# Optimization experiments

Measured on AMD Instinct MI355X. Metric: run time of the kernel, lower is better.

## Reference

```python
import jax, jax.numpy as jnp
import numpy as np

N_NODES = 50000
N_EDGES = 800000
F = 64      # node feature channels (irreps_out = 64x0e)
L = 4       # edge spherical-harmonic dim (lmax=1)
R = 8       # radial basis size
H = 64      # radial MLP hidden
AVG_NUM_NEIGHBOURS = 16.0


def setup_inputs() -> dict:
    key = jax.random.key(0)
    ks = jax.random.split(key, 10)
    node_features = jax.random.normal(ks[0], (N_NODES, F), jnp.float32)
    edge_features = jax.random.normal(ks[1], (N_EDGES, L), jnp.float32)
    radial_embedding = jax.random.uniform(ks[2], (N_EDGES, R), jnp.float32)
    senders = jax.random.randint(ks[3], (N_EDGES,), 0, N_NODES)
    receivers = jax.random.randint(ks[4], (N_EDGES,), 0, N_NODES)
    edge_mask = jnp.ones((N_EDGES,), jnp.bool_)
    W_up = jax.random.normal(ks[5], (F, F), jnp.float32) / np.sqrt(F)
    W1 = jax.random.normal(ks[6], (R, H), jnp.float32) / np.sqrt(R)
    W2 = jax.random.normal(ks[7], (H, H), jnp.float32) / np.sqrt(H)
    W3 = jax.random.normal(ks[8], (H, F * L), jnp.float32) / np.sqrt(H)
    W_down = jax.random.normal(ks[9], (F, F), jnp.float32) / np.sqrt(F)
    return dict(node_features=node_features, edge_features=edge_features,
                radial_embedding=radial_embedding, senders=senders,
                receivers=receivers, edge_mask=edge_mask,
                W_up=W_up, W1=W1, W2=W2, W3=W3, W_down=W_down)


def reference(node_features, edge_features, radial_embedding, senders,
              receivers, edge_mask, W_up, W1, W2, W3, W_down):
    n_nodes = node_features.shape[0]
    # linear_up
    x = node_features @ W_up  # [N, F]
    # radial MLP -> per-edge, per-(channel, l) tensor-product path weights
    h = jax.nn.swish(radial_embedding @ W1)
    h = jax.nn.swish(h @ W2)
    w = (h @ W3).reshape(-1, F, L)  # [E, F, L]
    # gather sender features, weighted tensor product with edge attrs,
    # contracted over the edge-attribute (spherical-harmonic) axis
    x_s = x[senders]  # [E, F]
    msg = jnp.einsum('ef,el,efl->ef', x_s, edge_features, w)  # [E, F]
    msg = jnp.where(edge_mask[:, None], msg, jnp.zeros((), msg.dtype))
    # scatter-add to receivers and normalize
    agg = jax.ops.segment_sum(msg, receivers, num_segments=n_nodes)
    agg = agg / AVG_NUM_NEIGHBOURS
    # linear_down
    return agg @ W_down
```

## Files before the change

kernel.cpp:

```cpp
#include <hip/hip_runtime.h>
#include <hip/hip_bf16.h>

typedef _Float16 half8 __attribute__((ext_vector_type(8)));
typedef _Float16 half4v __attribute__((ext_vector_type(4)));
typedef float f32x4 __attribute__((ext_vector_type(4)));

#define NN 50000
#define NE 800000

__device__ __forceinline__ float swishf(float v) {
  return v * __builtin_amdgcn_rcpf(1.f + __expf(-v));
}

__global__ __launch_bounds__(256)
void prep_kernel(const float* __restrict__ nf, const float* __restrict__ W_up,
                 _Float16* __restrict__ xbuf, const int* __restrict__ rcv,
                 int* __restrict__ deg, const float* __restrict__ W3,
                 const float* __restrict__ W2, _Float16* __restrict__ w3p,
                 _Float16* __restrict__ w2p) {
  const int b = blockIdx.x, tid = threadIdx.x;
  if (b < 12500) {
    const int gid = b * 256 + tid;
    const int row = gid >> 6, lane = tid & 63;
    const float* xr = nf + (long)row * 64;
    float acc = 0.f;
#pragma unroll
    for (int k = 0; k < 64; ++k) acc = fmaf(xr[k], W_up[k * 64 + lane], acc);
    xbuf[(long)row * 64 + lane] = (_Float16)acc;
  } else if (b < 15625) {
    const int e = (b - 12500) * 256 + tid;
    atomicAdd(&deg[rcv[e]], 1);
  } else {
    const int bb = b - 15625;
    if (bb < 8) {
      int t = bb * 256 + tid;
      int lane = t & 63, nt = (t >> 6) & 3, ks = t >> 8;
      int f = 16 * nt + (lane & 15);
      int jb = 32 * ks + 8 * (lane >> 4);
#pragma unroll
      for (int u = 0; u < 8; ++u) {
        int j = jb + u;
        w3p[t * 8 + u] = (_Float16)W3[(j >> 2) * 256 + 4 * f + (j & 3)];
      }
    } else {
      int t = (bb - 8) * 256 + tid;
      if (t < 512) {
        int lane = t & 63, nt = (t >> 6) & 3, kk = t >> 8;
        int c = 16 * nt + (lane & 15);
        int kb = 32 * kk + 8 * (lane >> 4);
#pragma unroll
        for (int u = 0; u < 8; ++u)
          w2p[t * 8 + u] = (_Float16)W2[(kb + u) * 64 + c];
      }
    }
  }
}

__global__ __launch_bounds__(256)
void scan1_kernel(const int* __restrict__ deg, int* __restrict__ bsum) {
  __shared__ int s[256];
  int gid = blockIdx.x * 256 + threadIdx.x;
  s[threadIdx.x] = (gid < NN) ? deg[gid] : 0;
  __syncthreads();
  for (int d = 128; d > 0; d >>= 1) {
    if (threadIdx.x < d) s[threadIdx.x] += s[threadIdx.x + d];
    __syncthreads();
  }
  if (threadIdx.x == 0) bsum[blockIdx.x] = s[0];
}

__global__ __launch_bounds__(256)
void scan2_kernel(const int* __restrict__ bsum, int* __restrict__ boff) {
  __shared__ int s[256];
  int t = threadIdx.x;
  int v = (t < 196) ? bsum[t] : 0;
  s[t] = v;
  __syncthreads();
  for (int d = 1; d < 256; d <<= 1) {
    int x = (t >= d) ? s[t - d] : 0;
    __syncthreads();
    s[t] += x;
    __syncthreads();
  }
  boff[t] = s[t] - v;
}

__global__ __launch_bounds__(256)
void scan3_kernel(const int* __restrict__ deg, const int* __restrict__ boff,
                  int* __restrict__ pos, int* __restrict__ cur) {
  __shared__ int s[256];
  int t = threadIdx.x, gid = blockIdx.x * 256 + t;
  int v = (gid < NN) ? deg[gid] : 0;
  s[t] = v;
  __syncthreads();
  for (int d = 1; d < 256; d <<= 1) {
    int x = (t >= d) ? s[t - d] : 0;
    __syncthreads();
    s[t] += x;
    __syncthreads();
  }
  int ex = s[t] - v + boff[blockIdx.x];
  if (gid < NN) {
    pos[gid] = ex;
    cur[gid] = ex;
    if (gid == NN - 1) pos[NN] = ex + v;
  }
}

__global__ __launch_bounds__(256, 4)
void fused_tp_kernel(const float* __restrict__ rad, const float* __restrict__ ef,
                     const _Float16* __restrict__ xup, const int* __restrict__ snd,
                     const int* __restrict__ rcv, const int* __restrict__ msk,
                     const float* __restrict__ W1,
                     const _Float16* __restrict__ w2p, const _Float16* __restrict__ w3p,
                     int* __restrict__ cur, _Float16* __restrict__ msg) {
  __shared__ float    s_ef[128][4];
  __shared__ _Float16 s_xs[128][72];
  __shared__ _Float16 s_hp[128][72];
  __shared__ int      s_slot[128];

  const int t = threadIdx.x;
  const long e0 = (long)blockIdx.x * 128;
  const int w = t >> 6, lane = t & 63, m = lane & 15, g = lane >> 4;
  const int ew0 = 32 * w;

  {
    const float2 e2 = *reinterpret_cast<const float2*>(ef + (e0 + ew0) * 4 + lane * 2);
    const int rr = ew0 + (lane >> 1), rc = 2 * (lane & 1);
    s_ef[rr][rc] = e2.x;
    s_ef[rr][rc + 1] = e2.y;
    if (lane < 32) s_slot[ew0 + lane] = atomicAdd(&cur[rcv[e0 + ew0 + lane]], 1);
    const int e = ew0 + (lane >> 1), q2 = lane & 1;
    const int sn = snd[e0 + e];
    const int mk = msk[e0 + e];
    uint4 v0 = {0,0,0,0}, v1 = {0,0,0,0}, v2 = {0,0,0,0}, v3 = {0,0,0,0};
    if (mk) {
      const uint4* src = reinterpret_cast<const uint4*>(xup + (long)sn * 64 + q2 * 32);
      v0 = src[0]; v1 = src[1]; v2 = src[2]; v3 = src[3];
    }
    uint4* dst = reinterpret_cast<uint4*>(&s_xs[e][q2 * 32]);
    dst[0] = v0; dst[1] = v1; dst[2] = v2; dst[3] = v3;
  }

  const int em0 = ew0 + m;
  const int em1 = ew0 + 16 + m;

  float rv0[8], rv1[8];
  {
    const float4 a = *reinterpret_cast<const float4*>(rad + (e0 + em0) * 8);
    const float4 b = *reinterpret_cast<const float4*>(rad + (e0 + em0) * 8 + 4);
    const float4 c = *reinterpret_cast<const float4*>(rad + (e0 + em1) * 8);
    const float4 d = *reinterpret_cast<const float4*>(rad + (e0 + em1) * 8 + 4);
    rv0[0]=a.x; rv0[1]=a.y; rv0[2]=a.z; rv0[3]=a.w;
    rv0[4]=b.x; rv0[5]=b.y; rv0[6]=b.z; rv0[7]=b.w;
    rv1[0]=c.x; rv1[1]=c.y; rv1[2]=c.z; rv1[3]=c.w;
    rv1[4]=d.x; rv1[5]=d.y; rv1[6]=d.z; rv1[7]=d.w;
  }

  half8 af0[2], af1[2];
#pragma unroll
  for (int kk = 0; kk < 2; ++kk) {
    float a0[8], a1[8];
#pragma unroll
    for (int u = 0; u < 8; ++u) { a0[u] = 0.f; a1[u] = 0.f; }
#pragma unroll
    for (int k = 0; k < 8; ++k) {
      const float4 wa = *reinterpret_cast<const float4*>(W1 + k * 64 + 32 * kk + 8 * g);
      const float4 wb = *reinterpret_cast<const float4*>(W1 + k * 64 + 32 * kk + 8 * g + 4);
      a0[0] = fmaf(rv0[k], wa.x, a0[0]);  a1[0] = fmaf(rv1[k], wa.x, a1[0]);
      a0[1] = fmaf(rv0[k], wa.y, a0[1]);  a1[1] = fmaf(rv1[k], wa.y, a1[1]);
      a0[2] = fmaf(rv0[k], wa.z, a0[2]);  a1[2] = fmaf(rv1[k], wa.z, a1[2]);
      a0[3] = fmaf(rv0[k], wa.w, a0[3]);  a1[3] = fmaf(rv1[k], wa.w, a1[3]);
      a0[4] = fmaf(rv0[k], wb.x, a0[4]);  a1[4] = fmaf(rv1[k], wb.x, a1[4]);
      a0[5] = fmaf(rv0[k], wb.y, a0[5]);  a1[5] = fmaf(rv1[k], wb.y, a1[5]);
      a0[6] = fmaf(rv0[k], wb.z, a0[6]);  a1[6] = fmaf(rv1[k], wb.z, a1[6]);
      a0[7] = fmaf(rv0[k], wb.w, a0[7]);  a1[7] = fmaf(rv1[k], wb.w, a1[7]);
    }
#pragma unroll
    for (int u = 0; u < 8; ++u) {
      af0[kk][u] = (_Float16)swishf(a0[u]);
      af1[kk][u] = (_Float16)swishf(a1[u]);
    }
  }

  {
    half8 bw[8];
#pragma unroll
    for (int i = 0; i < 8; ++i)
      bw[i] = *reinterpret_cast<const half8*>(w2p + ((size_t)i * 64 + lane) * 8);

    f32x4 A0[4], A1[4];
#pragma unroll
    for (int nt = 0; nt < 4; ++nt) { A0[nt] = (f32x4){0.f,0.f,0.f,0.f}; A1[nt] = (f32x4){0.f,0.f,0.f,0.f}; }
#pragma unroll
    for (int kk = 0; kk < 2; ++kk) {
#pragma unroll
      for (int nt = 0; nt < 4; ++nt) {
        A0[nt] = __builtin_amdgcn_mfma_f32_16x16x32_f16(af0[kk], bw[kk * 4 + nt], A0[nt], 0, 0, 0);
        A1[nt] = __builtin_amdgcn_mfma_f32_16x16x32_f16(af1[kk], bw[kk * 4 + nt], A1[nt], 0, 0, 0);
      }
    }
    const int col = lane & 15, rg = lane >> 4;
    const int pbase = 16 * ((col >> 1) & 3) + 2 * (col >> 3) + (col & 1);
#pragma unroll
    for (int nt = 0; nt < 4; ++nt) {
      const int pos = pbase + 4 * nt;
#pragma unroll
      for (int i = 0; i < 4; ++i) {
        const int r0 = ew0 + rg * 4 + i;
        s_hp[r0][pos]      = (_Float16)swishf(A0[nt][i]);
        s_hp[r0 + 16][pos] = (_Float16)swishf(A1[nt][i]);
      }
    }
  }

  {
    const _Float16* hr0 = &s_hp[em0][g * 16];
    const _Float16* hr1 = &s_hp[em1][g * 16];
    half8 hlo0 = *reinterpret_cast<const half8*>(hr0);
    half8 hhi0 = *reinterpret_cast<const half8*>(hr0 + 8);
    half8 hlo1 = *reinterpret_cast<const half8*>(hr1);
    half8 hhi1 = *reinterpret_cast<const half8*>(hr1 + 8);

    _Float16 ef0[4], ef1[4];
#pragma unroll
    for (int l = 0; l < 4; ++l) {
      ef0[l] = (_Float16)s_ef[em0][l];
      ef1[l] = (_Float16)s_ef[em1][l];
    }

    f32x4 c0[4], c1[4];
#pragma unroll
    for (int nt = 0; nt < 4; ++nt) { c0[nt] = (f32x4){0.f,0.f,0.f,0.f}; c1[nt] = (f32x4){0.f,0.f,0.f,0.f}; }

#pragma unroll
    for (int ks = 0; ks < 8; ++ks) {
      half8 bfr[4];
#pragma unroll
      for (int nt = 0; nt < 4; ++nt)
        bfr[nt] = *reinterpret_cast<const half8*>(w3p + ((size_t)(ks * 4 + nt) * 64 + lane) * 8);

      const _Float16 p0  = (ks < 4) ? hlo0[2 * ks]     : hhi0[2 * (ks - 4)];
      const _Float16 p1  = (ks < 4) ? hlo0[2 * ks + 1] : hhi0[2 * (ks - 4) + 1];
      const _Float16 q0  = (ks < 4) ? hlo1[2 * ks]     : hhi1[2 * (ks - 4)];
      const _Float16 q1  = (ks < 4) ? hlo1[2 * ks + 1] : hhi1[2 * (ks - 4) + 1];
      half8 a0, a1;
#pragma unroll
      for (int l = 0; l < 4; ++l) {
        a0[l]     = p0 * ef0[l];
        a0[4 + l] = p1 * ef0[l];
        a1[l]     = q0 * ef1[l];
        a1[4 + l] = q1 * ef1[l];
      }
#pragma unroll
      for (int nt = 0; nt < 4; ++nt) {
        c0[nt] = __builtin_amdgcn_mfma_f32_16x16x32_f16(a0, bfr[nt], c0[nt], 0, 0, 0);
        c1[nt] = __builtin_amdgcn_mfma_f32_16x16x32_f16(a1, bfr[nt], c1[nt], 0, 0, 0);
      }
    }

    const int col = lane & 15, rg = lane >> 4;
#pragma unroll
    for (int nt = 0; nt < 4; ++nt) {
      const int f = nt * 16 + col;
#pragma unroll
      for (int i = 0; i < 4; ++i) {
        const int r0 = ew0 + rg * 4 + i;
        s_hp[r0][f]      = (_Float16)(c0[nt][i] * (float)s_xs[r0][f]);
        s_hp[r0 + 16][f] = (_Float16)(c1[nt][i] * (float)s_xs[r0 + 16][f]);
      }
    }
  }

  {
    const int e = ew0 + (lane >> 1), q2 = lane & 1;
    const uint4* src = reinterpret_cast<const uint4*>(&s_hp[e][q2 * 32]);
    uint4 v0 = src[0], v1 = src[1], v2 = src[2], v3 = src[3];
    uint4* dst = reinterpret_cast<uint4*>(msg + (long)s_slot[e] * 64 + q2 * 32);
    dst[0] = v0; dst[1] = v1; dst[2] = v2; dst[3] = v3;
  }
}

__global__ __launch_bounds__(256, 8)
void gather_down_kernel(const _Float16* __restrict__ msg, const int* __restrict__ pos,
                        const float* __restrict__ W_dn, float* __restrict__ out) {
  __shared__ int   s_pos[17];
  __shared__ float s_agg[16][65];

  const int t = threadIdx.x;
  const int node0 = blockIdx.x * 16;

  if (t < 17) s_pos[t] = pos[node0 + t];
  __syncthreads();

  const int tg = t >> 4, tl = t & 15;
  float a0 = 0.f, a1 = 0.f, a2 = 0.f, a3 = 0.f;
  for (int a = s_pos[tg]; a < s_pos[tg + 1]; ++a) {
    half4v v = *reinterpret_cast<const half4v*>(msg + (long)a * 64 + tl * 4);
    a0 += (float)v[0]; a1 += (float)v[1]; a2 += (float)v[2]; a3 += (float)v[3];
  }
  s_agg[tg][tl * 4 + 0] = a0;
  s_agg[tg][tl * 4 + 1] = a1;
  s_agg[tg][tl * 4 + 2] = a2;
  s_agg[tg][tl * 4 + 3] = a3;
  __syncthreads();

  {
    const int r = t >> 4, c0 = (t & 15) * 4;
    float b0 = 0.f, b1 = 0.f, b2 = 0.f, b3 = 0.f;
    for (int k = 0; k < 64; ++k) {
      const float x = s_agg[r][k];
      const float4 wv = *reinterpret_cast<const float4*>(W_dn + k * 64 + c0);
      b0 = fmaf(x, wv.x, b0);
      b1 = fmaf(x, wv.y, b1);
      b2 = fmaf(x, wv.z, b2);
      b3 = fmaf(x, wv.w, b3);
    }
    float4 o = { b0 * 0.0625f, b1 * 0.0625f, b2 * 0.0625f, b3 * 0.0625f };
    *reinterpret_cast<float4*>(out + (long)(node0 + r) * 64 + c0) = o;
  }
}

extern "C" void kernel_launch(void* const* d_in, const int* in_sizes, int n_in,
                              void* d_out, int out_size, void* d_ws, size_t ws_size,
                              hipStream_t stream) {
  const float* nf   = (const float*)d_in[0];
  const float* ef   = (const float*)d_in[1];
  const float* rad  = (const float*)d_in[2];
  const int*   snd  = (const int*)d_in[3];
  const int*   rcv  = (const int*)d_in[4];
  const int*   msk  = (const int*)d_in[5];
  const float* W_up = (const float*)d_in[6];
  const float* W1   = (const float*)d_in[7];
  const float* W2   = (const float*)d_in[8];
  const float* W3   = (const float*)d_in[9];
  const float* W_dn = (const float*)d_in[10];
  float* out = (float*)d_out;

  _Float16* msg  = (_Float16*)d_ws;
  _Float16* xbuf = msg + (size_t)NE * 64;
  _Float16* w3p  = xbuf + (size_t)NN * 64;
  _Float16* w2p  = w3p + 2048 * 8;
  int*      deg  = (int*)(w2p + 512 * 8);
  int*      pos  = deg + NN;
  int*      cur  = pos + NN + 1;
  int*      bsum = cur + NN;
  int*      boff = bsum + 256;

  hipMemsetAsync(deg, 0, (size_t)NN * sizeof(int), stream);

  prep_kernel<<<15635, 256, 0, stream>>>(nf, W_up, xbuf, rcv, deg, W3, W2, w3p, w2p);

  scan1_kernel<<<196, 256, 0, stream>>>(deg, bsum);
  scan2_kernel<<<1, 256, 0, stream>>>(bsum, boff);
  scan3_kernel<<<196, 256, 0, stream>>>(deg, boff, pos, cur);

  fused_tp_kernel<<<NE / 128, 256, 0, stream>>>(rad, ef, xbuf, snd, rcv, msk,
                                                W1, w2p, w3p, cur, msg);

  gather_down_kernel<<<NN / 16, 256, 0, stream>>>(msg, pos, W_dn, out);
}
```

Measured before the change: 240.0 us.

## Replace CSR sort-and-gather aggregation with direct float atomics into node buffer

Removes the receiver degree count, three prefix-scan kernels, per-edge slot atomics, and the fp16 message buffer with its gather pass. Each edge's message element is instead atomically added into a zeroed fp32 per-node accumulator, followed by a simple linear_down kernel. This trades a large message write/read and several launches for many scalar float atomics. Summation order also becomes nondeterministic.

```diff
diff --git a/kernel.cpp b/kernel.cpp
--- a/kernel.cpp
+++ b/kernel.cpp
@@ -2,7 +2,6 @@
 #include <hip/hip_bf16.h>
 
 typedef _Float16 half8 __attribute__((ext_vector_type(8)));
-typedef _Float16 half4v __attribute__((ext_vector_type(4)));
 typedef float f32x4 __attribute__((ext_vector_type(4)));
 
 #define NN 50000
@@ -14,8 +13,7 @@
 
 __global__ __launch_bounds__(256)
 void prep_kernel(const float* __restrict__ nf, const float* __restrict__ W_up,
-                 _Float16* __restrict__ xbuf, const int* __restrict__ rcv,
-                 int* __restrict__ deg, const float* __restrict__ W3,
+                 _Float16* __restrict__ xbuf, const float* __restrict__ W3,
                  const float* __restrict__ W2, _Float16* __restrict__ w3p,
                  _Float16* __restrict__ w2p) {
   const int b = blockIdx.x, tid = threadIdx.x;
@@ -27,11 +25,8 @@
 #pragma unroll
     for (int k = 0; k < 64; ++k) acc = fmaf(xr[k], W_up[k * 64 + lane], acc);
     xbuf[(long)row * 64 + lane] = (_Float16)acc;
-  } else if (b < 15625) {
-    const int e = (b - 12500) * 256 + tid;
-    atomicAdd(&deg[rcv[e]], 1);
   } else {
-    const int bb = b - 15625;
+    const int bb = b - 12500;
     if (bb < 8) {
       int t = bb * 256 + tid;
       int lane = t & 63, nt = (t >> 6) & 3, ks = t >> 8;
@@ -57,54 +52,16 @@
 }
 
 __global__ __launch_bounds__(256)
-void scan1_kernel(const int* __restrict__ deg, int* __restrict__ bsum) {
-  __shared__ int s[256];
-  int gid = blockIdx.x * 256 + threadIdx.x;
-  s[threadIdx.x] = (gid < NN) ? deg[gid] : 0;
-  __syncthreads();
-  for (int d = 128; d > 0; d >>= 1) {
-    if (threadIdx.x < d) s[threadIdx.x] += s[threadIdx.x + d];
-    __syncthreads();
-  }
-  if (threadIdx.x == 0) bsum[blockIdx.x] = s[0];
-}
-
-__global__ __launch_bounds__(256)
-void scan2_kernel(const int* __restrict__ bsum, int* __restrict__ boff) {
-  __shared__ int s[256];
-  int t = threadIdx.x;
-  int v = (t < 196) ? bsum[t] : 0;
-  s[t] = v;
-  __syncthreads();
-  for (int d = 1; d < 256; d <<= 1) {
-    int x = (t >= d) ? s[t - d] : 0;
-    __syncthreads();
-    s[t] += x;
-    __syncthreads();
-  }
-  boff[t] = s[t] - v;
-}
-
-__global__ __launch_bounds__(256)
-void scan3_kernel(const int* __restrict__ deg, const int* __restrict__ boff,
-                  int* __restrict__ pos, int* __restrict__ cur) {
-  __shared__ int s[256];
-  int t = threadIdx.x, gid = blockIdx.x * 256 + t;
-  int v = (gid < NN) ? deg[gid] : 0;
-  s[t] = v;
-  __syncthreads();
-  for (int d = 1; d < 256; d <<= 1) {
-    int x = (t >= d) ? s[t - d] : 0;
-    __syncthreads();
-    s[t] += x;
-    __syncthreads();
-  }
-  int ex = s[t] - v + boff[blockIdx.x];
-  if (gid < NN) {
-    pos[gid] = ex;
-    cur[gid] = ex;
-    if (gid == NN - 1) pos[NN] = ex + v;
-  }
+void linear_down_kernel(const float* __restrict__ X, const float* __restrict__ W,
+                        float* __restrict__ Y) {
+  int gid = blockIdx.x * 256 + (int)threadIdx.x;
+  int row = gid >> 6;
+  int lane = threadIdx.x & 63;
+  const float* xr = X + (long)row * 64;
+  float acc = 0.f;
+#pragma unroll
+  for (int k = 0; k < 64; ++k) acc = fmaf(xr[k], W[k * 64 + lane], acc);
+  Y[(long)row * 64 + lane] = acc * 0.0625f;
 }
 
 __global__ __launch_bounds__(256, 4)
@@ -113,11 +70,10 @@
                      const int* __restrict__ rcv, const int* __restrict__ msk,
                      const float* __restrict__ W1,
                      const _Float16* __restrict__ w2p, const _Float16* __restrict__ w3p,
-                     int* __restrict__ cur, _Float16* __restrict__ msg) {
+                     float* __restrict__ agg) {
   __shared__ float    s_ef[128][4];
   __shared__ _Float16 s_xs[128][72];
   __shared__ _Float16 s_hp[128][72];
-  __shared__ int      s_slot[128];
 
   const int t = threadIdx.x;
   const long e0 = (long)blockIdx.x * 128;
@@ -129,7 +85,6 @@
     const int rr = ew0 + (lane >> 1), rc = 2 * (lane & 1);
     s_ef[rr][rc] = e2.x;
     s_ef[rr][rc + 1] = e2.y;
-    if (lane < 32) s_slot[ew0 + lane] = atomicAdd(&cur[rcv[e0 + ew0 + lane]], 1);
     const int e = ew0 + (lane >> 1), q2 = lane & 1;
     const int sn = snd[e0 + e];
     const int mk = msk[e0 + e];
@@ -260,64 +215,24 @@
     }
 
     const int col = lane & 15, rg = lane >> 4;
+    int rc0[4], rc1[4];
+#pragma unroll
+    for (int i = 0; i < 4; ++i) {
+      rc0[i] = rcv[e0 + ew0 + rg * 4 + i];
+      rc1[i] = rcv[e0 + ew0 + 16 + rg * 4 + i];
+    }
 #pragma unroll
     for (int nt = 0; nt < 4; ++nt) {
       const int f = nt * 16 + col;
 #pragma unroll
       for (int i = 0; i < 4; ++i) {
         const int r0 = ew0 + rg * 4 + i;
-        s_hp[r0][f]      = (_Float16)(c0[nt][i] * (float)s_xs[r0][f]);
-        s_hp[r0 + 16][f] = (_Float16)(c1[nt][i] * (float)s_xs[r0 + 16][f]);
-      }
-    }
-  }
-
-  {
-    const int e = ew0 + (lane >> 1), q2 = lane & 1;
-    const uint4* src = reinterpret_cast<const uint4*>(&s_hp[e][q2 * 32]);
-    uint4 v0 = src[0], v1 = src[1], v2 = src[2], v3 = src[3];
-    uint4* dst = reinterpret_cast<uint4*>(msg + (long)s_slot[e] * 64 + q2 * 32);
-    dst[0] = v0; dst[1] = v1; dst[2] = v2; dst[3] = v3;
-  }
-}
-
-__global__ __launch_bounds__(256, 8)
-void gather_down_kernel(const _Float16* __restrict__ msg, const int* __restrict__ pos,
-                        const float* __restrict__ W_dn, float* __restrict__ out) {
-  __shared__ int   s_pos[17];
-  __shared__ float s_agg[16][65];
-
-  const int t = threadIdx.x;
-  const int node0 = blockIdx.x * 16;
-
-  if (t < 17) s_pos[t] = pos[node0 + t];
-  __syncthreads();
-
-  const int tg = t >> 4, tl = t & 15;
-  float a0 = 0.f, a1 = 0.f, a2 = 0.f, a3 = 0.f;
-  for (int a = s_pos[tg]; a < s_pos[tg + 1]; ++a) {
-    half4v v = *reinterpret_cast<const half4v*>(msg + (long)a * 64 + tl * 4);
-    a0 += (float)v[0]; a1 += (float)v[1]; a2 += (float)v[2]; a3 += (float)v[3];
-  }
-  s_agg[tg][tl * 4 + 0] = a0;
-  s_agg[tg][tl * 4 + 1] = a1;
-  s_agg[tg][tl * 4 + 2] = a2;
-  s_agg[tg][tl * 4 + 3] = a3;
-  __syncthreads();
-
-  {
-    const int r = t >> 4, c0 = (t & 15) * 4;
-    float b0 = 0.f, b1 = 0.f, b2 = 0.f, b3 = 0.f;
-    for (int k = 0; k < 64; ++k) {
-      const float x = s_agg[r][k];
-      const float4 wv = *reinterpret_cast<const float4*>(W_dn + k * 64 + c0);
-      b0 = fmaf(x, wv.x, b0);
-      b1 = fmaf(x, wv.y, b1);
-      b2 = fmaf(x, wv.z, b2);
-      b3 = fmaf(x, wv.w, b3);
-    }
-    float4 o = { b0 * 0.0625f, b1 * 0.0625f, b2 * 0.0625f, b3 * 0.0625f };
-    *reinterpret_cast<float4*>(out + (long)(node0 + r) * 64 + c0) = o;
+        const float v0 = c0[nt][i] * (float)s_xs[r0][f];
+        const float v1 = c1[nt][i] * (float)s_xs[r0 + 16][f];
+        unsafeAtomicAdd(&agg[(size_t)rc0[i] * 64 + f], v0);
+        unsafeAtomicAdd(&agg[(size_t)rc1[i] * 64 + f], v1);
+      }
+    }
   }
 }
 
@@ -337,26 +252,17 @@
   const float* W_dn = (const float*)d_in[10];
   float* out = (float*)d_out;
 
-  _Float16* msg  = (_Float16*)d_ws;
-  _Float16* xbuf = msg + (size_t)NE * 64;
+  float*    agg  = (float*)d_ws;
+  _Float16* xbuf = (_Float16*)(agg + (size_t)NN * 64);
   _Float16* w3p  = xbuf + (size_t)NN * 64;
   _Float16* w2p  = w3p + 2048 * 8;
-  int*      deg  = (int*)(w2p + 512 * 8);
-  int*      pos  = deg + NN;
-  int*      cur  = pos + NN + 1;
-  int*      bsum = cur + NN;
-  int*      boff = bsum + 256;
-
-  hipMemsetAsync(deg, 0, (size_t)NN * sizeof(int), stream);
-
-  prep_kernel<<<15635, 256, 0, stream>>>(nf, W_up, xbuf, rcv, deg, W3, W2, w3p, w2p);
-
-  scan1_kernel<<<196, 256, 0, stream>>>(deg, bsum);
-  scan2_kernel<<<1, 256, 0, stream>>>(bsum, boff);
-  scan3_kernel<<<196, 256, 0, stream>>>(deg, boff, pos, cur);
+
+  hipMemsetAsync(agg, 0, (size_t)NN * 64 * sizeof(float), stream);
+
+  prep_kernel<<<12510, 256, 0, stream>>>(nf, W_up, xbuf, W3, W2, w3p, w2p);
 
   fused_tp_kernel<<<NE / 128, 256, 0, stream>>>(rad, ef, xbuf, snd, rcv, msk,
-                                                W1, w2p, w3p, cur, msg);
-
-  gather_down_kernel<<<NN / 16, 256, 0, stream>>>(msg, pos, W_dn, out);
-}
+                                                W1, w2p, w3p, agg);
+
+  linear_down_kernel<<<(NN * 64) / 256, 256, 0, stream>>>(agg, W_dn, out);
+}
```

Result: slower. 292.1 us (+21.7%).
